# Kernel optimization log

Hardware: AMD Instinct MI355X
Metric: run time of the kernel (lower is better)

The kernel has to match this reference:

```python
import jax, jax.numpy as jnp
import numpy as np
from jax.scipy.special import logsumexp

D_MODEL = 512
NHEAD = 8
BATCH = 2
SEQ = 1024


def _safe_log_relu(v):
    # log(max(v, 0)) with well-defined (zero) gradient where v <= 0
    pos = v > 0
    return jnp.where(pos, jnp.log(jnp.where(pos, v, 1.0)), -jnp.inf)


def _split_heads(t, h):
    b, l, hd = t.shape
    return t.reshape(b, l, h, hd // h).transpose(0, 2, 1, 3)  # (B,H,L,d)


def setup_inputs() -> dict:
    key = jax.random.key(0)
    ks = jax.random.split(key, 9)
    s = 1.0 / np.sqrt(D_MODEL)
    x = jax.random.normal(ks[0], (BATCH, SEQ, D_MODEL), jnp.float32)
    mk = lambda k: jax.random.normal(k, (D_MODEL, D_MODEL), jnp.float32) * s
    mb = lambda k: jax.random.normal(k, (D_MODEL,), jnp.float32) * 0.02
    return {
        "x": x,
        "W_Q": mk(ks[1]), "b_Q": mb(ks[2]),
        "W_K": mk(ks[3]), "b_K": mb(ks[4]),
        "W_V": mk(ks[5]), "b_V": mb(ks[6]),
        "W_O": mk(ks[7]), "b_O": mb(ks[8]),
    }


def reference(x, W_Q, b_Q, W_K, b_K, W_V, b_V, W_O, b_O):
    # self-attention: queries = keys = values = x
    Q = _split_heads(x @ W_Q.T + b_Q, NHEAD)  # (B,H,L,D)
    K = _split_heads(x @ W_K.T + b_K, NHEAD)  # (B,H,L,D)
    V = _split_heads(x @ W_V.T + b_V, NHEAD)  # (B,H,L,Dv)

    # normalizer: log sum_j sum_d exp(Q_id) * exp(K_jd)
    log_B = logsumexp(Q + logsumexp(K, axis=-2, keepdims=True), axis=-1)  # (B,H,L)

    log_V_plus = _safe_log_relu(V)[..., None, :]    # (B,H,L,1,Dv)
    log_V_minus = _safe_log_relu(-V)[..., None, :]  # (B,H,L,1,Dv)

    # reduce over key positions: (B,H,L,D,Dv) -> (B,H,D,Dv)
    lse_KV_plus = logsumexp(K[..., :, :, None] + log_V_plus, axis=-3)
    lse_KV_minus = logsumexp(K[..., :, :, None] + log_V_minus, axis=-3)

    # reduce over feature dim D: (B,H,L,D,Dv) -> (B,H,L,Dv)
    log_A_plus = logsumexp(Q[..., None] + lse_KV_plus[..., None, :, :], axis=-2)
    log_A_minus = logsumexp(Q[..., None] + lse_KV_minus[..., None, :, :], axis=-2)

    heads = jnp.exp(log_A_plus - log_B[..., None]) - jnp.exp(log_A_minus - log_B[..., None])

    b, h, l, dv = heads.shape
    joined = heads.transpose(0, 2, 1, 3).reshape(b, l, h * dv)
    return joined @ W_O.T + b_O
```

## Files before the change

### kernel.cpp

```cpp
#include <hip/hip_runtime.h>
#include <math.h>

#define DM   512
#define NH   8
#define HD   64
#define B_   2
#define L_   1024
#define M_   (B_ * L_)

typedef __attribute__((ext_vector_type(8))) short  bfrag;
typedef __attribute__((ext_vector_type(4))) float  fv4;
typedef __attribute__((ext_vector_type(4))) unsigned short usv4;

__device__ __forceinline__ unsigned short f32_bf16_rne(float f) {
    unsigned u = __float_as_uint(f);
    unsigned r = u + 0x7FFF + ((u >> 16) & 1);
    return (unsigned short)(r >> 16);
}
__device__ __forceinline__ float bf16_f32(unsigned short h) {
    return __uint_as_float(((unsigned)h) << 16);
}

__device__ __forceinline__ void stage16(const unsigned short* g, unsigned short* l) {
    __builtin_amdgcn_global_load_lds(
        (const __attribute__((address_space(1))) void*)g,
        (__attribute__((address_space(3))) void*)l,
        16, 0, 0);
}

__global__ __launch_bounds__(256) void prep_kernel(
    const float* __restrict__ x,
    const float* __restrict__ Wq, const float* __restrict__ Wk,
    const float* __restrict__ Wv, const float* __restrict__ Wo,
    unsigned short* __restrict__ xh, unsigned short* __restrict__ xl,
    unsigned short* __restrict__ wh, unsigned short* __restrict__ wl) {
    int bid = blockIdx.x;
    const float* src; unsigned short *dh, *dl; size_t off;
    if (bid < 1024) {
        src = x; dh = xh; dl = xl; off = (size_t)bid * 1024;
    } else {
        int wsel = (bid - 1024) >> 8;
        int wb   = (bid - 1024) & 255;
        src = (wsel == 0) ? Wq : (wsel == 1) ? Wk : (wsel == 2) ? Wv : Wo;
        dh = wh + (size_t)wsel * 262144;
        dl = wl + (size_t)wsel * 262144;
        off = (size_t)wb * 1024;
    }
    size_t i = off + (size_t)threadIdx.x * 4;
    float4 v = *(const float4*)(src + i);
    usv4 h, l;
    h.x = f32_bf16_rne(v.x); l.x = f32_bf16_rne(v.x - bf16_f32(h.x));
    h.y = f32_bf16_rne(v.y); l.y = f32_bf16_rne(v.y - bf16_f32(h.y));
    h.z = f32_bf16_rne(v.z); l.z = f32_bf16_rne(v.z - bf16_f32(h.z));
    h.w = f32_bf16_rne(v.w); l.w = f32_bf16_rne(v.w - bf16_f32(h.w));
    *(usv4*)(dh + i) = h;
    *(usv4*)(dl + i) = l;
}

#define TM 128
#define TN 64
#define TK 32
#define LDA 32

__device__ __forceinline__ void mfma_gemm_bf16(
    const unsigned short* __restrict__ Ahg, const unsigned short* __restrict__ Alg,
    const unsigned short* __restrict__ Bhg, const unsigned short* __restrict__ Blg,
    const float* __restrict__ bias, float* __restrict__ C, int do_exp) {
    __shared__ __align__(16) unsigned short Ah[TM * LDA];
    __shared__ __align__(16) unsigned short Al[TM * LDA];
    __shared__ __align__(16) unsigned short Bh[TN * LDA];
    __shared__ __align__(16) unsigned short Bl[TN * LDA];

    const int tid  = threadIdx.x;
    const int wave = tid >> 6, lane = tid & 63;
    const int quad = lane >> 4, r16 = lane & 15;
    const int m0 = blockIdx.y * TM, n0 = blockIdx.x * TN;

    const int srow = lane >> 2;
    const int scol = (lane & 3) << 3;

    fv4 acc[2][4] = {};

    for (int k0 = 0; k0 < DM; k0 += TK) {
        {
            const int c1 = wave, c2 = wave + 4;
            size_t ga1 = (size_t)(m0 + c1 * 16 + srow) * DM + k0 + scol;
            size_t ga2 = (size_t)(m0 + c2 * 16 + srow) * DM + k0 + scol;
            stage16(Ahg + ga1, Ah + c1 * 512);
            stage16(Ahg + ga2, Ah + c2 * 512);
            stage16(Alg + ga1, Al + c1 * 512);
            stage16(Alg + ga2, Al + c2 * 512);
            size_t gb = (size_t)(n0 + c1 * 16 + srow) * DM + k0 + scol;
            stage16(Bhg + gb, Bh + c1 * 512);
            stage16(Blg + gb, Bl + c1 * 512);
        }
        __syncthreads();

        bfrag ah[2], al[2], bh[4], bl[4];
#pragma unroll
        for (int i = 0; i < 2; ++i) {
            int off = (wave * 32 + i * 16 + r16) * LDA + quad * 8;
            ah[i] = *(const bfrag*)(Ah + off);
            al[i] = *(const bfrag*)(Al + off);
        }
#pragma unroll
        for (int j = 0; j < 4; ++j) {
            int off = (j * 16 + r16) * LDA + quad * 8;
            bh[j] = *(const bfrag*)(Bh + off);
            bl[j] = *(const bfrag*)(Bl + off);
        }

#pragma unroll
        for (int i = 0; i < 2; ++i)
#pragma unroll
            for (int j = 0; j < 4; ++j) {
                acc[i][j] = __builtin_amdgcn_mfma_f32_16x16x32_bf16(ah[i], bh[j], acc[i][j], 0, 0, 0);
                acc[i][j] = __builtin_amdgcn_mfma_f32_16x16x32_bf16(ah[i], bl[j], acc[i][j], 0, 0, 0);
                acc[i][j] = __builtin_amdgcn_mfma_f32_16x16x32_bf16(al[i], bh[j], acc[i][j], 0, 0, 0);
            }
        __syncthreads();
    }

#pragma unroll
    for (int j = 0; j < 4; ++j) {
        int n = n0 + j * 16 + r16;
        float bn = bias[n];
#pragma unroll
        for (int i = 0; i < 2; ++i) {
#pragma unroll
            for (int r = 0; r < 4; ++r) {
                int m = m0 + wave * 32 + i * 16 + quad * 4 + r;
                float v = acc[i][j][r] + bn;
                if (do_exp) v = __expf(v);
                C[(size_t)m * DM + n] = v;
            }
        }
    }
}

__global__ __launch_bounds__(256) void gemm_qkv_kernel(
    const unsigned short* __restrict__ xh, const unsigned short* __restrict__ xl,
    const unsigned short* __restrict__ wh, const unsigned short* __restrict__ wl,
    const float* __restrict__ bq, const float* __restrict__ bk, const float* __restrict__ bv,
    float* __restrict__ Qe, float* __restrict__ Ke, float* __restrict__ V) {
    int z = blockIdx.z;
    const float* b = (z == 0) ? bq : (z == 1) ? bk : bv;
    float* C = (z == 0) ? Qe : (z == 1) ? Ke : V;
    mfma_gemm_bf16(xh, xl, wh + (size_t)z * 262144, wl + (size_t)z * 262144,
                   b, C, z < 2);
}

__global__ __launch_bounds__(256) void gemm_out_kernel(
    const unsigned short* __restrict__ jh, const unsigned short* __restrict__ jl,
    const unsigned short* __restrict__ wh, const unsigned short* __restrict__ wl,
    const float* __restrict__ bo, float* __restrict__ C) {
    mfma_gemm_bf16(jh, jl, wh + (size_t)3 * 262144, wl + (size_t)3 * 262144,
                   bo, C, 0);
}

#define JT 64
__global__ __launch_bounds__(256) void kv_stats_kernel(
    const float* __restrict__ Kbuf, const float* __restrict__ Vbuf,
    float* __restrict__ Spart, float* __restrict__ zpart) {
    const int split = blockIdx.x, bh = blockIdx.y;
    const int b = bh >> 3, h = bh & 7;
    const int j0 = split * JT;

    __shared__ __align__(16) float EK[JT][HD + 4];
    __shared__ __align__(16) float VS[JT][HD + 4];

    const int tid = threadIdx.x;
#pragma unroll
    for (int t = 0; t < 4; ++t) {
        int idx = tid + t * 256;
        int r = idx >> 4;
        int c = (idx & 15) << 2;
        size_t row = (size_t)(b * L_ + j0 + r) * DM + h * HD + c;
        *(float4*)&EK[r][c] = *(const float4*)(Kbuf + row);
        *(float4*)&VS[r][c] = *(const float4*)(Vbuf + row);
    }
    __syncthreads();

    const int tx = tid & 15, ty = tid >> 4;
    float acc[4][4] = {{0.f}};
#pragma unroll 8
    for (int jj = 0; jj < JT; ++jj) {
        float4 ek = *(const float4*)&EK[jj][ty * 4];
        float4 vs = *(const float4*)&VS[jj][tx * 4];
        float e[4] = {ek.x, ek.y, ek.z, ek.w};
        float v[4] = {vs.x, vs.y, vs.z, vs.w};
#pragma unroll
        for (int i = 0; i < 4; ++i)
#pragma unroll
            for (int j = 0; j < 4; ++j) acc[i][j] += e[i] * v[j];
    }

    float* sp = Spart + ((size_t)bh * 16 + split) * (HD * HD);
#pragma unroll
    for (int i = 0; i < 4; ++i) {
        float4 o; o.x = acc[i][0]; o.y = acc[i][1]; o.z = acc[i][2]; o.w = acc[i][3];
        *(float4*)(sp + (ty * 4 + i) * HD + tx * 4) = o;
    }
    if (tid < HD) {
        float z = 0.f;
#pragma unroll 8
        for (int jj = 0; jj < JT; ++jj) z += EK[jj][tid];
        zpart[((size_t)bh * 16 + split) * HD + tid] = z;
    }
}

__global__ __launch_bounds__(256) void heads_kernel(
    const float* __restrict__ Qbuf, const float* __restrict__ Spart,
    const float* __restrict__ zpart,
    unsigned short* __restrict__ jh, unsigned short* __restrict__ jl) {
    const int tileI = blockIdx.x, bh = blockIdx.y;
    const int b = bh >> 3, h = bh & 7;

    __shared__ __align__(16) float S[HD][HD + 4];
    __shared__ float zl[HD];

    const int tid = threadIdx.x;
#pragma unroll
    for (int t = 0; t < 4; ++t) {
        int idx4 = tid + t * 256;
        const float* sp = Spart + (size_t)bh * 16 * (HD * HD) + (size_t)idx4 * 4;
        float4 s = {0.f, 0.f, 0.f, 0.f};
#pragma unroll
        for (int p = 0; p < 16; ++p) {
            float4 v = *(const float4*)(sp + (size_t)p * (HD * HD));
            s.x += v.x; s.y += v.y; s.z += v.z; s.w += v.w;
        }
        int row = idx4 >> 4, col = (idx4 & 15) << 2;
        *(float4*)&S[row][col] = s;
    }
    if (tid < HD) {
        float z = 0.f;
        const float* zp = zpart + (size_t)bh * 16 * HD + tid;
#pragma unroll
        for (int p = 0; p < 16; ++p) z += zp[(size_t)p * HD];
        zl[tid] = z;
    }
    __syncthreads();

    const int lane = tid & 63, w = tid >> 6;
#pragma unroll 1
    for (int r = 0; r < 16; ++r) {
        int i = tileI * 64 + w * 16 + r;
        float eq = Qbuf[(size_t)(b * L_ + i) * DM + h * HD + lane];

        float denom = eq * zl[lane];
#pragma unroll
        for (int off = 32; off; off >>= 1) denom += __shfl_xor(denom, off, 64);

        float acc = 0.f;
#pragma unroll
        for (int d = 0; d < HD; ++d) {
            float bq = __shfl(eq, d, 64);
            acc += bq * S[d][lane];
        }
        float val = acc / denom;
        size_t oidx = (size_t)(b * L_ + i) * DM + h * HD + lane;
        unsigned short hh = f32_bf16_rne(val);
        unsigned short ll = f32_bf16_rne(val - bf16_f32(hh));
        jh[oidx] = hh;
        jl[oidx] = ll;
    }
}

extern "C" void kernel_launch(void* const* d_in, const int* in_sizes, int n_in,
                              void* d_out, int out_size, void* d_ws, size_t ws_size,
                              hipStream_t stream) {
    const float* x  = (const float*)d_in[0];
    const float* Wq = (const float*)d_in[1];
    const float* bq = (const float*)d_in[2];
    const float* Wk = (const float*)d_in[3];
    const float* bk = (const float*)d_in[4];
    const float* Wv = (const float*)d_in[5];
    const float* bv = (const float*)d_in[6];
    const float* Wo = (const float*)d_in[7];
    const float* bo = (const float*)d_in[8];
    float* out = (float*)d_out;

    float* f = (float*)d_ws;
    const size_t NQ = (size_t)M_ * DM;
    float* Qe    = f;
    float* Ke    = f + NQ;
    float* V     = f + 2 * NQ;
    float* Spart = f + 3 * NQ;
    float* zpart = f + 4 * NQ;
    unsigned short* u = (unsigned short*)(f + 4 * NQ + 16384);
    unsigned short* xh = u;
    unsigned short* xl = u + NQ;
    unsigned short* wh = u + 2 * NQ;
    unsigned short* wl = u + 3 * NQ;
    unsigned short* jh = u + 4 * NQ;
    unsigned short* jl = u + 5 * NQ;

    prep_kernel<<<2048, 256, 0, stream>>>(x, Wq, Wk, Wv, Wo, xh, xl, wh, wl);

    dim3 gQKV(DM / TN, M_ / TM, 3);
    gemm_qkv_kernel<<<gQKV, 256, 0, stream>>>(xh, xl, wh, wl, bq, bk, bv, Qe, Ke, V);

    kv_stats_kernel<<<dim3(16, 16), 256, 0, stream>>>(Ke, V, Spart, zpart);

    heads_kernel<<<dim3(16, 16), 256, 0, stream>>>(Qe, Spart, zpart, jh, jl);

    dim3 gO(DM / TN, M_ / TM, 1);
    gemm_out_kernel<<<gO, 256, 0, stream>>>(jh, jl, wh, wl, bo, out);
}
```

Baseline: 140.6 us.

## Fold the KV summary into per-batch output weights and simplify the heads stage

Reassociates the attention output so each batch's KV summary S_h is multiplied into W_O first. This gives a per-batch 512x512 weight W2, and the out-projection GEMM then reads normalized exp(Q) directly. The per-row 64x64 mat-vec in the old heads kernel is replaced by an elementwise divide-and-split pass, plus a small W2-building stage in the same mid kernel. The key-sum partials are now reduced with atomics into a buffer zeroed by an extra prep block, and W_O is no longer split in prep. The out GEMM now reads different weights for each batch, and the order of floating-point summation changes.

```diff
diff --git a/kernel.cpp b/kernel.cpp
--- a/kernel.cpp
+++ b/kernel.cpp
@@ -11,6 +11,7 @@
 typedef __attribute__((ext_vector_type(8))) short  bfrag;
 typedef __attribute__((ext_vector_type(4))) float  fv4;
 typedef __attribute__((ext_vector_type(4))) unsigned short usv4;
+typedef __attribute__((ext_vector_type(8))) unsigned short usv8;
 
 __device__ __forceinline__ unsigned short f32_bf16_rne(float f) {
     unsigned u = __float_as_uint(f);
@@ -31,17 +32,23 @@
 __global__ __launch_bounds__(256) void prep_kernel(
     const float* __restrict__ x,
     const float* __restrict__ Wq, const float* __restrict__ Wk,
-    const float* __restrict__ Wv, const float* __restrict__ Wo,
+    const float* __restrict__ Wv,
     unsigned short* __restrict__ xh, unsigned short* __restrict__ xl,
-    unsigned short* __restrict__ wh, unsigned short* __restrict__ wl) {
+    unsigned short* __restrict__ wh, unsigned short* __restrict__ wl,
+    float* __restrict__ zred) {
     int bid = blockIdx.x;
+    if (bid >= 1792) {
+        float4 zv = {0.f, 0.f, 0.f, 0.f};
+        *(float4*)(zred + (size_t)threadIdx.x * 4) = zv;
+        return;
+    }
     const float* src; unsigned short *dh, *dl; size_t off;
     if (bid < 1024) {
         src = x; dh = xh; dl = xl; off = (size_t)bid * 1024;
     } else {
         int wsel = (bid - 1024) >> 8;
         int wb   = (bid - 1024) & 255;
-        src = (wsel == 0) ? Wq : (wsel == 1) ? Wk : (wsel == 2) ? Wv : Wo;
+        src = (wsel == 0) ? Wq : (wsel == 1) ? Wk : Wv;
         dh = wh + (size_t)wsel * 262144;
         dl = wl + (size_t)wsel * 262144;
         off = (size_t)wb * 1024;
@@ -152,16 +159,17 @@
 
 __global__ __launch_bounds__(256) void gemm_out_kernel(
     const unsigned short* __restrict__ jh, const unsigned short* __restrict__ jl,
-    const unsigned short* __restrict__ wh, const unsigned short* __restrict__ wl,
+    const unsigned short* __restrict__ w2h, const unsigned short* __restrict__ w2l,
     const float* __restrict__ bo, float* __restrict__ C) {
-    mfma_gemm_bf16(jh, jl, wh + (size_t)3 * 262144, wl + (size_t)3 * 262144,
+    int b = blockIdx.y >> 3;
+    mfma_gemm_bf16(jh, jl, w2h + (size_t)b * 262144, w2l + (size_t)b * 262144,
                    bo, C, 0);
 }
 
 #define JT 64
 __global__ __launch_bounds__(256) void kv_stats_kernel(
     const float* __restrict__ Kbuf, const float* __restrict__ Vbuf,
-    float* __restrict__ Spart, float* __restrict__ zpart) {
+    float* __restrict__ Spart, float* __restrict__ zred) {
     const int split = blockIdx.x, bh = blockIdx.y;
     const int b = bh >> 3, h = bh & 7;
     const int j0 = split * JT;
@@ -205,65 +213,100 @@
         float z = 0.f;
 #pragma unroll 8
         for (int jj = 0; jj < JT; ++jj) z += EK[jj][tid];
-        zpart[((size_t)bh * 16 + split) * HD + tid] = z;
-    }
-}
-
-__global__ __launch_bounds__(256) void heads_kernel(
-    const float* __restrict__ Qbuf, const float* __restrict__ Spart,
-    const float* __restrict__ zpart,
+        atomicAdd(zred + (size_t)bh * HD + tid, z);
+    }
+}
+
+__global__ __launch_bounds__(256) void mid_kernel(
+    const float* __restrict__ Spart, const float* __restrict__ zred,
+    const float* __restrict__ Qbuf, const float* __restrict__ Wo,
+    unsigned short* __restrict__ w2h, unsigned short* __restrict__ w2l,
     unsigned short* __restrict__ jh, unsigned short* __restrict__ jl) {
-    const int tileI = blockIdx.x, bh = blockIdx.y;
-    const int b = bh >> 3, h = bh & 7;
-
-    __shared__ __align__(16) float S[HD][HD + 4];
-    __shared__ float zl[HD];
-
     const int tid = threadIdx.x;
-#pragma unroll
-    for (int t = 0; t < 4; ++t) {
-        int idx4 = tid + t * 256;
-        const float* sp = Spart + (size_t)bh * 16 * (HD * HD) + (size_t)idx4 * 4;
-        float4 s = {0.f, 0.f, 0.f, 0.f};
-#pragma unroll
-        for (int p = 0; p < 16; ++p) {
-            float4 v = *(const float4*)(sp + (size_t)p * (HD * HD));
-            s.x += v.x; s.y += v.y; s.z += v.z; s.w += v.w;
-        }
-        int row = idx4 >> 4, col = (idx4 & 15) << 2;
-        *(float4*)&S[row][col] = s;
-    }
-    if (tid < HD) {
-        float z = 0.f;
-        const float* zp = zpart + (size_t)bh * 16 * HD + tid;
-#pragma unroll
-        for (int p = 0; p < 16; ++p) z += zp[(size_t)p * HD];
-        zl[tid] = z;
-    }
-    __syncthreads();
-
-    const int lane = tid & 63, w = tid >> 6;
-#pragma unroll 1
-    for (int r = 0; r < 16; ++r) {
-        int i = tileI * 64 + w * 16 + r;
-        float eq = Qbuf[(size_t)(b * L_ + i) * DM + h * HD + lane];
-
-        float denom = eq * zl[lane];
-#pragma unroll
-        for (int off = 32; off; off >>= 1) denom += __shfl_xor(denom, off, 64);
-
-        float acc = 0.f;
-#pragma unroll
-        for (int d = 0; d < HD; ++d) {
-            float bq = __shfl(eq, d, 64);
-            acc += bq * S[d][lane];
-        }
-        float val = acc / denom;
-        size_t oidx = (size_t)(b * L_ + i) * DM + h * HD + lane;
-        unsigned short hh = f32_bf16_rne(val);
-        unsigned short ll = f32_bf16_rne(val - bf16_f32(hh));
-        jh[oidx] = hh;
-        jl[oidx] = ll;
+    const int bid = blockIdx.x;
+    if (bid < 128) {
+        __shared__ __align__(16) float Sl[HD][HD + 4];
+        __shared__ __align__(16) float Wol[HD][HD + 4];
+        const int b = bid >> 6, r = bid & 63;
+        const int h = r >> 3, nq = r & 7;
+        const int n0 = nq * 64, bh = b * NH + h;
+        const float* sp = Spart + (size_t)bh * 16 * (HD * HD);
+#pragma unroll
+        for (int t4 = 0; t4 < 4; ++t4) {
+            int idx4 = tid + t4 * 256;
+            const float* p0 = sp + (size_t)idx4 * 4;
+            float4 s = {0.f, 0.f, 0.f, 0.f};
+#pragma unroll
+            for (int p = 0; p < 16; ++p) {
+                float4 v = *(const float4*)(p0 + (size_t)p * (HD * HD));
+                s.x += v.x; s.y += v.y; s.z += v.z; s.w += v.w;
+            }
+            int d = idx4 >> 4, e4 = (idx4 & 15) << 2;
+            *(float4*)&Sl[d][e4] = s;
+            *(float4*)&Wol[d][e4] =
+                *(const float4*)(Wo + (size_t)(n0 + d) * DM + h * HD + e4);
+        }
+        __syncthreads();
+        const int nl = tid & 15;
+        const int d0 = tid >> 4;
+        float acc[4][4] = {};
+#pragma unroll
+        for (int e4 = 0; e4 < 16; ++e4) {
+            float4 w[4], s[4];
+#pragma unroll
+            for (int j = 0; j < 4; ++j) w[j] = *(const float4*)&Wol[nl + j * 16][e4 * 4];
+#pragma unroll
+            for (int i = 0; i < 4; ++i) s[i] = *(const float4*)&Sl[d0 + i * 16][e4 * 4];
+#pragma unroll
+            for (int j = 0; j < 4; ++j)
+#pragma unroll
+                for (int i = 0; i < 4; ++i)
+                    acc[j][i] += w[j].x * s[i].x + w[j].y * s[i].y
+                               + w[j].z * s[i].z + w[j].w * s[i].w;
+        }
+#pragma unroll
+        for (int j = 0; j < 4; ++j) {
+            int n = n0 + nl + j * 16;
+#pragma unroll
+            for (int i = 0; i < 4; ++i) {
+                int d = d0 + i * 16;
+                size_t addr = ((size_t)(b * DM + n)) * DM + h * HD + d;
+                float v = acc[j][i];
+                unsigned short hh = f32_bf16_rne(v);
+                w2h[addr] = hh;
+                w2l[addr] = f32_bf16_rne(v - bf16_f32(hh));
+            }
+        }
+    } else {
+        const int bid2 = bid - 128;
+        const int w = tid >> 6, lane = tid & 63;
+        const int b = bid2 >> 5;
+        const int row0 = bid2 * 32 + w * 8;
+        const float4 z0 = *(const float4*)(zred + (size_t)b * DM + lane * 8);
+        const float4 z1 = *(const float4*)(zred + (size_t)b * DM + lane * 8 + 4);
+#pragma unroll
+        for (int rr = 0; rr < 8; ++rr) {
+            const size_t rowoff = (size_t)(row0 + rr) * DM + lane * 8;
+            float4 q0 = *(const float4*)(Qbuf + rowoff);
+            float4 q1 = *(const float4*)(Qbuf + rowoff + 4);
+            float part = q0.x * z0.x + q0.y * z0.y + q0.z * z0.z + q0.w * z0.w
+                       + q1.x * z1.x + q1.y * z1.y + q1.z * z1.z + q1.w * z1.w;
+            part += __shfl_xor(part, 1, 64);
+            part += __shfl_xor(part, 2, 64);
+            part += __shfl_xor(part, 4, 64);
+            float inv = 1.0f / part;
+            float v[8] = {q0.x * inv, q0.y * inv, q0.z * inv, q0.w * inv,
+                          q1.x * inv, q1.y * inv, q1.z * inv, q1.w * inv};
+            usv8 hv, lv;
+#pragma unroll
+            for (int k = 0; k < 8; ++k) {
+                unsigned short hh = f32_bf16_rne(v[k]);
+                hv[k] = hh;
+                lv[k] = f32_bf16_rne(v[k] - bf16_f32(hh));
+            }
+            *(usv8*)(jh + rowoff) = hv;
+            *(usv8*)(jl + rowoff) = lv;
+        }
     }
 }
 
@@ -287,24 +330,26 @@
     float* Ke    = f + NQ;
     float* V     = f + 2 * NQ;
     float* Spart = f + 3 * NQ;
-    float* zpart = f + 4 * NQ;
-    unsigned short* u = (unsigned short*)(f + 4 * NQ + 16384);
-    unsigned short* xh = u;
-    unsigned short* xl = u + NQ;
-    unsigned short* wh = u + 2 * NQ;
-    unsigned short* wl = u + 3 * NQ;
-    unsigned short* jh = u + 4 * NQ;
-    unsigned short* jl = u + 5 * NQ;
-
-    prep_kernel<<<2048, 256, 0, stream>>>(x, Wq, Wk, Wv, Wo, xh, xl, wh, wl);
+    float* zred  = f + 4 * NQ;
+    unsigned short* u = (unsigned short*)(f + 4 * NQ + 1024);
+    unsigned short* xh  = u;
+    unsigned short* xl  = u + NQ;
+    unsigned short* wh  = u + 2 * NQ;
+    unsigned short* wl  = u + 2 * NQ + 786432;
+    unsigned short* jh  = u + 2 * NQ + 2 * 786432;
+    unsigned short* jl  = jh + NQ;
+    unsigned short* w2h = jl + NQ;
+    unsigned short* w2l = w2h + 524288;
+
+    prep_kernel<<<1793, 256, 0, stream>>>(x, Wq, Wk, Wv, xh, xl, wh, wl, zred);
 
     dim3 gQKV(DM / TN, M_ / TM, 3);
     gemm_qkv_kernel<<<gQKV, 256, 0, stream>>>(xh, xl, wh, wl, bq, bk, bv, Qe, Ke, V);
 
-    kv_stats_kernel<<<dim3(16, 16), 256, 0, stream>>>(Ke, V, Spart, zpart);
-
-    heads_kernel<<<dim3(16, 16), 256, 0, stream>>>(Qe, Spart, zpart, jh, jl);
+    kv_stats_kernel<<<dim3(16, 16), 256, 0, stream>>>(Ke, V, Spart, zred);
+
+    mid_kernel<<<192, 256, 0, stream>>>(Spart, zred, Qe, Wo, w2h, w2l, jh, jl);
 
     dim3 gO(DM / TN, M_ / TM, 1);
-    gemm_out_kernel<<<gO, 256, 0, stream>>>(jh, jl, wh, wl, bo, out);
-}
+    gemm_out_kernel<<<gO, 256, 0, stream>>>(jh, jl, w2h, w2l, bo, out);
+}
```

Result: faster. 130.6 us (-7.1%).
